# Optimization experiments

Measured on AMD Instinct MI355X. Metric: run time of the kernel, lower is better.

Reference implementation:

```python
import jax, jax.numpy as jnp
import numpy as np


def _sobel_mag(x_bchw):
    # per-channel Sobel gradient magnitude, then mean over channels -> [B,1,H,W]
    B, C, H, W = x_bchw.shape
    kx = jnp.array([[-1, 0, 1], [-2, 0, 2], [-1, 0, 1]], dtype=x_bchw.dtype).reshape(1, 1, 3, 3)
    ky = jnp.array([[-1, -2, -1], [0, 0, 0], [1, 2, 1]], dtype=x_bchw.dtype).reshape(1, 1, 3, 3)
    xf = x_bchw.reshape(B * C, 1, H, W)
    dn = ('NCHW', 'OIHW', 'NCHW')
    gx = jax.lax.conv_general_dilated(xf, kx, (1, 1), 'SAME', dimension_numbers=dn)
    gy = jax.lax.conv_general_dilated(xf, ky, (1, 1), 'SAME', dimension_numbers=dn)
    mag = jnp.sqrt(gx * gx + gy * gy + 1e-8).reshape(B, C, H, W)
    return mag.mean(axis=1, keepdims=True)


def _bi_wkv(w, u, k, v):
    # Bidirectional WKV (Vision-RWKV):
    # y_t = (sum_{i!=t} exp(k_i - (|t-i|-1)*w) v_i + exp(u+k_t) v_t)
    #     / (sum_{i!=t} exp(k_i - (|t-i|-1)*w)     + exp(u+k_t))
    # w,u: [C];  k,v: [B,T,C]. Numerically stable prefix scans in both directions.
    B, T, C = k.shape
    kt = jnp.transpose(k, (1, 0, 2))  # [T,B,C]
    vt = jnp.transpose(v, (1, 0, 2))

    def scan_dir(ks, vs):
        def step(carry, kv):
            a, b, pp = carry  # running num, den at log-offset pp (exclusive prefix)
            kk, vv = kv
            out = (a, b, pp)
            ww = pp - w  # decay one step
            p = jnp.maximum(ww, kk)
            e1 = jnp.exp(ww - p)
            e2 = jnp.exp(kk - p)
            return (e1 * a + e2 * vv, e1 * b + e2, p), out
        init = (jnp.zeros((B, C), k.dtype), jnp.zeros((B, C), k.dtype),
                jnp.full((B, C), -1e38, k.dtype))
        _, (a, b, pp) = jax.lax.scan(step, init, (ks, vs))
        return a, b, pp

    af, bf, pf = scan_dir(kt, vt)                       # contributions i < t
    ab, bb, pb = scan_dir(kt[::-1], vt[::-1])           # contributions i > t
    ab, bb, pb = ab[::-1], bb[::-1], pb[::-1]

    ps = u + kt                                         # self term exponent
    m = jnp.maximum(jnp.maximum(pf, pb), ps)
    ef = jnp.exp(pf - m)
    eb = jnp.exp(pb - m)
    es = jnp.exp(ps - m)
    num = af * ef + ab * eb + es * vt
    den = bf * ef + bb * eb + es
    return jnp.transpose(num / den, (1, 0, 2))  # [B,T,C]


def setup_inputs() -> dict:
    key = jax.random.key(0)
    ks = jax.random.split(key, 8)
    B, H, W, C = 8, 64, 64, 256
    T = H * W
    s = 1.0 / np.sqrt(C)
    return {
        'x': jax.random.normal(ks[0], (B, T, C), jnp.float32),
        'Wk': jax.random.normal(ks[1], (C, C), jnp.float32) * s,
        'Wv': jax.random.normal(ks[2], (C, C), jnp.float32) * s,
        'Wr': jax.random.normal(ks[3], (C, C), jnp.float32) * s,
        'Wo': jax.random.normal(ks[4], (C, C), jnp.float32) * s,
        'spatial_decay': jax.random.uniform(ks[5], (C,), jnp.float32, 0.5, 1.5),
        'spatial_first': jax.random.uniform(ks[6], (C,), jnp.float32, 0.5, 1.5),
        'H': H,
        'W': W,
    }


def reference(x, Wk, Wv, Wr, Wo, spatial_decay, spatial_first, H, W):
    B, T, C = x.shape
    k = x @ Wk.T
    v = x @ Wv.T
    r = x @ Wr.T
    sr = jax.nn.sigmoid(r)
    # edge gate
    x_hw = jnp.transpose(x, (0, 2, 1)).reshape(B, C, H, W)
    edge_g = jax.nn.sigmoid(_sobel_mag(x_hw)).reshape(B, 1, T)
    sr = sr + jnp.transpose(edge_g, (0, 2, 1))
    # bi-directional WKV with w,u scaled by 1/T (as in forward)
    xwkv = _bi_wkv(spatial_decay / T, spatial_first / T, k, v)
    return (sr * xwkv) @ Wo.T
```

## Files before the change

kernel.cpp:

```cpp
#include <hip/hip_runtime.h>
#include <hip/hip_bf16.h>

#define TB 8
#define TT 4096
#define TC 256
#define NC2 128
#define CL2 32

typedef _Float16 half8 __attribute__((ext_vector_type(8)));
typedef _Float16 half4v __attribute__((ext_vector_type(4)));
typedef float floatx4 __attribute__((ext_vector_type(4)));

#define GLDS16(g, l) __builtin_amdgcn_global_load_lds( \
    (const __attribute__((address_space(1))) void*)(g), \
    (__attribute__((address_space(3))) void*)(l), 16, 0, 0)

__global__ __launch_bounds__(256) void prep(
    const float* __restrict__ x,
    const float* __restrict__ Wk, const float* __restrict__ Wv,
    const float* __restrict__ Wr, const float* __restrict__ Wo,
    _Float16* __restrict__ Xh, _Float16* __restrict__ Xl,
    _Float16* __restrict__ Wf, float* __restrict__ edge)
{
    if (blockIdx.x >= TB * TT) {
        int t4 = (blockIdx.x - TB * TT) * 256 + threadIdx.x;
        int f = t4 * 4;
        int wsel = f >> 16;
        int i = f & 65535;
        const float* src = (wsel == 0) ? Wk : (wsel == 1) ? Wv :
                           (wsel == 2) ? Wr : Wo;
        float4 v = *(const float4*)(src + i);
        half4v h;
        h.x = (_Float16)v.x; h.y = (_Float16)v.y;
        h.z = (_Float16)v.z; h.w = (_Float16)v.w;
        *(half4v*)(Wf + (size_t)wsel * 65536 + i) = h;
        return;
    }
    int t = blockIdx.x & (TT - 1);
    int b = blockIdx.x >> 12;
    int h = t >> 6, w = t & 63;
    int c = threadIdx.x;

    float n[3][3];
    #pragma unroll
    for (int dh = 0; dh < 3; dh++) {
        int hh = h + dh - 1;
        #pragma unroll
        for (int dw = 0; dw < 3; dw++) {
            int ww = w + dw - 1;
            float val = 0.f;
            if (hh >= 0 && hh < 64 && ww >= 0 && ww < 64)
                val = x[((size_t)(b * TT + (hh << 6) + ww)) * TC + c];
            n[dh][dw] = val;
        }
    }
    float xc = n[1][1];
    _Float16 hi = (_Float16)xc;
    _Float16 lo = (_Float16)(xc - (float)hi);
    size_t mi = (size_t)(b * TT + t) * TC + c;
    Xh[mi] = hi;
    Xl[mi] = lo;

    float gx = (n[0][2] - n[0][0]) + 2.f * (n[1][2] - n[1][0]) + (n[2][2] - n[2][0]);
    float gy = (n[2][0] + 2.f * n[2][1] + n[2][2]) - (n[0][0] + 2.f * n[0][1] + n[0][2]);
    float mag = sqrtf(gx * gx + gy * gy + 1e-8f);

    #pragma unroll
    for (int off = 32; off > 0; off >>= 1) mag += __shfl_down(mag, off, 64);
    __shared__ float part[4];
    if ((threadIdx.x & 63) == 0) part[threadIdx.x >> 6] = mag;
    __syncthreads();
    if (threadIdx.x == 0) {
        float s = part[0] + part[1] + part[2] + part[3];
        edge[blockIdx.x] = 1.f / (1.f + __expf(-s * (1.f / 256.f)));
    }
}

__global__ __launch_bounds__(256, 2) void gemm_split(
    const _Float16* __restrict__ Ah_g, const _Float16* __restrict__ Al_g,
    const _Float16* __restrict__ W0, const _Float16* __restrict__ W1,
    const _Float16* __restrict__ W2p,
    void* __restrict__ C0, void* __restrict__ C1, void* __restrict__ C2,
    int ops)
{
    __shared__ __align__(16) _Float16 smem[16384];
    _Float16* Ah = smem;
    _Float16* Al = smem + 4096;
    _Float16* Bs = smem + 8192;

    int wsel = blockIdx.y;
    const _Float16* W = (wsel == 0) ? W0 : (wsel == 1) ? W1 : W2p;
    void* Cc          = (wsel == 0) ? C0 : (wsel == 1) ? C1 : C2;
    int op = (ops >> (2 * wsel)) & 3;
    int row0 = blockIdx.x * 128;

    int tid = threadIdx.x;
    int lane = tid & 63;
    int wv = tid >> 6;
    int qm = (wv >> 1) * 64;
    int qn = (wv & 1) * 128;

    floatx4 acc[4][8];
    #pragma unroll
    for (int i = 0; i < 4; i++)
        #pragma unroll
        for (int j = 0; j < 8; j++)
            acc[i][j] = (floatx4){0.f, 0.f, 0.f, 0.f};

    for (int kb = 0; kb < 256; kb += 32) {
        __syncthreads();
        #pragma unroll
        for (int r = 0; r < 2; r++) {
            int q = r * 256 + tid;
            int row = q >> 2;
            int s = q & 3;
            int g = (s - row - (row >> 2)) & 3;
            size_t goff = (size_t)(row0 + row) * TC + kb + g * 8;
            GLDS16(Ah_g + goff, &Ah[q * 8]);
            GLDS16(Al_g + goff, &Al[q * 8]);
        }
        #pragma unroll
        for (int r = 0; r < 4; r++) {
            int q = r * 256 + tid;
            int row = q >> 2, s = q & 3;
            int g = (s - row - (row >> 2)) & 3;
            GLDS16(W + (size_t)row * TC + kb + g * 8, &Bs[q * 8]);
        }
        __syncthreads();
        int sl = lane >> 4;
        half8 ah[4], al[4], b[8];
        #pragma unroll
        for (int i = 0; i < 4; i++) {
            int ra = qm + i * 16 + (lane & 15);
            int sa = (sl + ra + (ra >> 2)) & 3;
            ah[i] = *(const half8*)&Ah[ra * 32 + sa * 8];
            al[i] = *(const half8*)&Al[ra * 32 + sa * 8];
        }
        #pragma unroll
        for (int j = 0; j < 8; j++) {
            int rb = qn + j * 16 + (lane & 15);
            int sb = (sl + rb + (rb >> 2)) & 3;
            b[j] = *(const half8*)&Bs[rb * 32 + sb * 8];
        }
        #pragma unroll
        for (int i = 0; i < 4; i++)
            #pragma unroll
            for (int j = 0; j < 8; j++) {
                acc[i][j] = __builtin_amdgcn_mfma_f32_16x16x32_f16(
                    ah[i], b[j], acc[i][j], 0, 0, 0);
                acc[i][j] = __builtin_amdgcn_mfma_f32_16x16x32_f16(
                    al[i], b[j], acc[i][j], 0, 0, 0);
            }
    }

    int mr0 = (lane >> 4) * 4;
    int nc = lane & 15;
    #pragma unroll
    for (int i = 0; i < 4; i++) {
        #pragma unroll
        for (int r = 0; r < 4; r++) {
            int m = row0 + qm + i * 16 + mr0 + r;
            if (op == 0) {
                float* crow = (float*)Cc + (size_t)m * TC + qn + nc;
                #pragma unroll
                for (int j = 0; j < 8; j++)
                    crow[j * 16] = acc[i][j][r];
            } else {
                _Float16* crow = (_Float16*)Cc + (size_t)m * TC + qn + nc;
                #pragma unroll
                for (int j = 0; j < 8; j++) {
                    float vv = acc[i][j][r];
                    if (op == 1) vv = 1.f / (1.f + __expf(-vv));
                    else if (op == 2) vv = __expf(vv);
                    crow[j * 16] = (_Float16)vv;
                }
            }
        }
    }
}

__global__ __launch_bounds__(256) void wkv_chunk_sums(
    const _Float16* __restrict__ ekp, const _Float16* __restrict__ vp,
    const float* __restrict__ decay,
    float* __restrict__ SaF, float* __restrict__ SbF,
    float* __restrict__ RaB, float* __restrict__ RbB)
{
    int tid = blockIdx.x * 256 + threadIdx.x;
    int c = tid & 255;
    int j = (tid >> 8) & (NC2 - 1);
    int b = tid >> 15;
    float w = decay[c] * (1.f / (float)TT);
    float d = __expf(-w);
    size_t base = ((size_t)(b * TT + j * CL2)) * TC + c;
    float Sa = 0.f, Sb = 0.f, Ra = 0.f, Rb = 0.f, pw = 1.f;
    #pragma unroll
    for (int i = 0; i < CL2; i++) {
        float ek = (float)ekp[base + (size_t)i * TC];
        float vv = (float)vp[base + (size_t)i * TC];
        float ekv = ek * vv;
        Sa = fmaf(d, Sa, ekv);
        Sb = fmaf(d, Sb, ek);
        Ra = fmaf(pw, ekv, Ra);
        Rb = fmaf(pw, ek, Rb);
        pw *= d;
    }
    int idx = (b * NC2 + j) * TC + c;
    SaF[idx] = Sa; SbF[idx] = Sb; RaB[idx] = Ra; RbB[idx] = Rb;
}

__global__ __launch_bounds__(256) void wkv_carries(
    const float* __restrict__ SaF, const float* __restrict__ SbF,
    const float* __restrict__ RaB, const float* __restrict__ RbB,
    const float* __restrict__ decay,
    float* __restrict__ CfA, float* __restrict__ CfB,
    float* __restrict__ CbA, float* __restrict__ CbB)
{
    int gw = (blockIdx.x * 256 + threadIdx.x) >> 6;
    int lane = threadIdx.x & 63;
    int c = gw & 255, b = gw >> 8;
    float w = decay[c] * (1.f / (float)TT);
    float D = __expf(-(float)CL2 * w);
    int base = b * NC2 * TC + c;
    int j0 = 2 * lane, j1 = 2 * lane + 1;
    int r0 = NC2 - 1 - j0, r1 = NC2 - 2 - j0;

    float sa0 = SaF[base + j0 * TC], sa1 = SaF[base + j1 * TC];
    float sb0 = SbF[base + j0 * TC], sb1 = SbF[base + j1 * TC];
    float qa0 = RaB[base + r0 * TC], qa1 = RaB[base + r1 * TC];
    float qb0 = RbB[base + r0 * TC], qb1 = RbB[base + r1 * TC];

    float pa = fmaf(D, sa0, sa1), pb = fmaf(D, sb0, sb1);
    float ra = fmaf(D, qa0, qa1), rb = fmaf(D, qb0, qb1);

    float dp = D * D;
    #pragma unroll
    for (int off = 1; off < 64; off <<= 1) {
        float ta = __shfl_up(pa, off, 64);
        float tb = __shfl_up(pb, off, 64);
        float ua = __shfl_up(ra, off, 64);
        float ub = __shfl_up(rb, off, 64);
        if (lane >= off) {
            pa = fmaf(dp, ta, pa); pb = fmaf(dp, tb, pb);
            ra = fmaf(dp, ua, ra); rb = fmaf(dp, ub, rb);
        }
        dp = dp * dp;
    }
    float ppa = __shfl_up(pa, 1, 64);
    float ppb = __shfl_up(pb, 1, 64);
    float pra = __shfl_up(ra, 1, 64);
    float prb = __shfl_up(rb, 1, 64);
    if (lane == 0) { ppa = 0.f; ppb = 0.f; pra = 0.f; prb = 0.f; }

    CfA[base + j0 * TC] = ppa;
    CfA[base + j1 * TC] = fmaf(D, ppa, sa0);
    CfB[base + j0 * TC] = ppb;
    CfB[base + j1 * TC] = fmaf(D, ppb, sb0);
    CbA[base + r0 * TC] = pra;
    CbA[base + r1 * TC] = fmaf(D, pra, qa0);
    CbB[base + r0 * TC] = prb;
    CbB[base + r1 * TC] = fmaf(D, prb, qb0);
}

__global__ __launch_bounds__(256) void wkv_combine(
    const _Float16* __restrict__ ekp, const _Float16* __restrict__ vp,
    const _Float16* __restrict__ srp, const float* __restrict__ edgep,
    const float* __restrict__ decay, const float* __restrict__ first,
    const float* __restrict__ CfA, const float* __restrict__ CfB,
    const float* __restrict__ CbA, const float* __restrict__ CbB,
    _Float16* __restrict__ Yh, _Float16* __restrict__ Yl)
{
    __shared__ _Float16 ekL[CL2 * 256];
    __shared__ float ekvL[CL2 * 256];
    int bid = blockIdx.x;
    int j = bid & (NC2 - 1);
    int b = bid >> 7;
    int c = threadIdx.x;

    float w = decay[c] * (1.f / (float)TT);
    float d = __expf(-w);
    float eu = __expf(first[c] * (1.f / (float)TT));
    int cidx = (b * NC2 + j) * TC + c;
    size_t base = ((size_t)(b * TT + j * CL2)) * TC + c;

    float abArr[CL2], bbArr[CL2];
    float ab = CbA[cidx], bb = CbB[cidx];
    #pragma unroll
    for (int i = CL2 - 1; i >= 0; i--) {
        _Float16 ekh16 = ekp[base + (size_t)i * TC];
        float ek = (float)ekh16;
        float vv = (float)vp[base + (size_t)i * TC];
        float ekv = ek * vv;
        ekL[i * 256 + c] = ekh16;
        ekvL[i * 256 + c] = ekv;
        abArr[i] = ab; bbArr[i] = bb;
        ab = fmaf(d, ab, ekv);
        bb = fmaf(d, bb, ek);
    }
    float af = CfA[cidx], bf = CfB[cidx];
    #pragma unroll
    for (int i = 0; i < CL2; i++) {
        size_t idx = base + (size_t)i * TC;
        float ek = (float)ekL[i * 256 + c];
        float ekv = ekvL[i * 256 + c];
        float srv = (float)srp[idx];
        float num = fmaf(eu, ekv, af + abArr[i]);
        float den = fmaf(eu, ek, bf + bbArr[i]);
        float ev = edgep[b * TT + j * CL2 + i];
        float yv = (srv + ev) * (num / den);
        _Float16 yh = (_Float16)yv;
        _Float16 yl = (_Float16)(yv - (float)yh);
        Yh[idx] = yh;
        Yl[idx] = yl;
        af = fmaf(d, af, ekv);
        bf = fmaf(d, bf, ek);
    }
}

extern "C" void kernel_launch(void* const* d_in, const int* in_sizes, int n_in,
                              void* d_out, int out_size, void* d_ws, size_t ws_size,
                              hipStream_t stream)
{
    const float* x      = (const float*)d_in[0];
    const float* Wk     = (const float*)d_in[1];
    const float* Wv     = (const float*)d_in[2];
    const float* Wr     = (const float*)d_in[3];
    const float* Wo     = (const float*)d_in[4];
    const float* sdecay = (const float*)d_in[5];
    const float* sfirst = (const float*)d_in[6];
    float* out = (float*)d_out;

    char* ws = (char*)d_ws;
    size_t off = 0;
    const size_t PH = (size_t)TB * TT * TC * sizeof(_Float16);
    _Float16* Xh  = (_Float16*)(ws + off); off += PH;
    _Float16* Xl  = (_Float16*)(ws + off); off += PH;
    _Float16* ekh = (_Float16*)(ws + off); off += PH;
    _Float16* vbuf  = (_Float16*)(ws + off); off += PH;
    _Float16* srbuf = (_Float16*)(ws + off); off += PH;
    _Float16* Wf = (_Float16*)(ws + off); off += (size_t)4 * TC * TC * sizeof(_Float16);
    float* edge  = (float*)(ws + off); off += (size_t)TB * TT * sizeof(float);
    const size_t CHB = (size_t)TB * NC2 * TC * sizeof(float);
    float* SaF = (float*)(ws + off); off += CHB;
    float* SbF = (float*)(ws + off); off += CHB;
    float* RaB = (float*)(ws + off); off += CHB;
    float* RbB = (float*)(ws + off); off += CHB;
    float* CfA = (float*)(ws + off); off += CHB;
    float* CfB = (float*)(ws + off); off += CHB;
    float* CbA = (float*)(ws + off); off += CHB;
    float* CbB = (float*)(ws + off); off += CHB;

    _Float16* WfK = Wf;
    _Float16* WfV = Wf + (size_t)TC * TC;
    _Float16* WfR = Wf + (size_t)2 * TC * TC;
    _Float16* WfO = Wf + (size_t)3 * TC * TC;

    prep<<<TB * TT + 256, 256, 0, stream>>>(x, Wk, Wv, Wr, Wo, Xh, Xl, Wf, edge);

    int ops1 = 2 | (3 << 2) | (1 << 4);
    gemm_split<<<dim3((TB * TT) / 128, 3), 256, 0, stream>>>(
        Xh, Xl, WfK, WfV, WfR, ekh, vbuf, srbuf, ops1);

    wkv_chunk_sums<<<(TB * NC2 * TC) / 256, 256, 0, stream>>>(
        ekh, vbuf, sdecay, SaF, SbF, RaB, RbB);
    wkv_carries<<<(TB * TC * 64) / 256, 256, 0, stream>>>(
        SaF, SbF, RaB, RbB, sdecay, CfA, CfB, CbA, CbB);
    wkv_combine<<<TB * NC2, 256, 0, stream>>>(
        ekh, vbuf, srbuf, edge, sdecay, sfirst, CfA, CfB, CbA, CbB, Xh, Xl);

    gemm_split<<<dim3((TB * TT) / 128, 1), 256, 0, stream>>>(
        Xh, Xl, WfO, WfO, WfO, out, out, out, 0);
}
```

Before: 215.1 us.

## Split output GEMM into N=128 tiles, fold edge gate into sigmoid epilogue

Adds a dedicated output-projection GEMM kernel that covers 128 output columns per block, launched over two column halves. This doubles the block count and halves the accumulator registers and shared memory per block, aiming at better occupancy and wave coverage. The edge-gate addition moves into the sigmoid epilogue of the first GEMM. wkv_combine now keeps v in shared memory as fp16 and recomputes ek*v instead of storing it as fp32, which halves that LDS buffer. Adding edge before the fp16 rounding of sr slightly changes numerics.

```diff
diff --git a/kernel.cpp b/kernel.cpp
--- a/kernel.cpp
+++ b/kernel.cpp
@@ -81,7 +81,7 @@
     const _Float16* __restrict__ W0, const _Float16* __restrict__ W1,
     const _Float16* __restrict__ W2p,
     void* __restrict__ C0, void* __restrict__ C1, void* __restrict__ C2,
-    int ops)
+    const float* __restrict__ edgep, int ops)
 {
     __shared__ __align__(16) _Float16 smem[16384];
     _Float16* Ah = smem;
@@ -160,21 +160,96 @@
         #pragma unroll
         for (int r = 0; r < 4; r++) {
             int m = row0 + qm + i * 16 + mr0 + r;
-            if (op == 0) {
-                float* crow = (float*)Cc + (size_t)m * TC + qn + nc;
-                #pragma unroll
-                for (int j = 0; j < 8; j++)
-                    crow[j * 16] = acc[i][j][r];
-            } else {
-                _Float16* crow = (_Float16*)Cc + (size_t)m * TC + qn + nc;
-                #pragma unroll
-                for (int j = 0; j < 8; j++) {
-                    float vv = acc[i][j][r];
-                    if (op == 1) vv = 1.f / (1.f + __expf(-vv));
-                    else if (op == 2) vv = __expf(vv);
-                    crow[j * 16] = (_Float16)vv;
-                }
+            _Float16* crow = (_Float16*)Cc + (size_t)m * TC + qn + nc;
+            float ev = (op == 1) ? edgep[m] : 0.f;
+            #pragma unroll
+            for (int j = 0; j < 8; j++) {
+                float vv = acc[i][j][r];
+                if (op == 1) vv = 1.f / (1.f + __expf(-vv)) + ev;
+                else if (op == 2) vv = __expf(vv);
+                crow[j * 16] = (_Float16)vv;
             }
+        }
+    }
+}
+
+__global__ __launch_bounds__(256, 2) void gemm_n128(
+    const _Float16* __restrict__ Ah_g, const _Float16* __restrict__ Al_g,
+    const _Float16* __restrict__ W, float* __restrict__ C)
+{
+    __shared__ __align__(16) _Float16 smem[12288];
+    _Float16* Ah = smem;
+    _Float16* Al = smem + 4096;
+    _Float16* Bs = smem + 8192;
+
+    int col0 = (blockIdx.y & 1) * 128;
+    int row0 = blockIdx.x * 128;
+    const _Float16* Bg = W + (size_t)col0 * TC;
+
+    int tid = threadIdx.x;
+    int lane = tid & 63;
+    int wv = tid >> 6;
+    int qm = (wv >> 1) * 64;
+    int qn = (wv & 1) * 64;
+
+    floatx4 acc[4][4];
+    #pragma unroll
+    for (int i = 0; i < 4; i++)
+        #pragma unroll
+        for (int j = 0; j < 4; j++)
+            acc[i][j] = (floatx4){0.f, 0.f, 0.f, 0.f};
+
+    for (int kb = 0; kb < 256; kb += 32) {
+        __syncthreads();
+        #pragma unroll
+        for (int r = 0; r < 2; r++) {
+            int q = r * 256 + tid;
+            int row = q >> 2;
+            int s = q & 3;
+            int g = (s - row - (row >> 2)) & 3;
+            size_t goff = (size_t)(row0 + row) * TC + kb + g * 8;
+            GLDS16(Ah_g + goff, &Ah[q * 8]);
+            GLDS16(Al_g + goff, &Al[q * 8]);
+            GLDS16(Bg + (size_t)row * TC + kb + g * 8, &Bs[q * 8]);
+        }
+        __syncthreads();
+        int sl = lane >> 4;
+        half8 ah[4], al[4], b[4];
+        #pragma unroll
+        for (int i = 0; i < 4; i++) {
+            int ra = qm + i * 16 + (lane & 15);
+            int sa = (sl + ra + (ra >> 2)) & 3;
+            ah[i] = *(const half8*)&Ah[ra * 32 + sa * 8];
+            al[i] = *(const half8*)&Al[ra * 32 + sa * 8];
+        }
+        #pragma unroll
+        for (int j = 0; j < 4; j++) {
+            int rb = qn + j * 16 + (lane & 15);
+            int sb = (sl + rb + (rb >> 2)) & 3;
+            b[j] = *(const half8*)&Bs[rb * 32 + sb * 8];
+        }
+        #pragma unroll
+        for (int i = 0; i < 4; i++)
+            #pragma unroll
+            for (int j = 0; j < 4; j++) {
+                acc[i][j] = __builtin_amdgcn_mfma_f32_16x16x32_f16(
+                    ah[i], b[j], acc[i][j], 0, 0, 0);
+                acc[i][j] = __builtin_amdgcn_mfma_f32_16x16x32_f16(
+                    al[i], b[j], acc[i][j], 0, 0, 0);
+            }
+    }
+
+    int mr0 = (lane >> 4) * 4;
+    int nc = lane & 15;
+    #pragma unroll
+    for (int i = 0; i < 4; i++) {
+        #pragma unroll
+        for (int r = 0; r < 4; r++) {
+            int m = row0 + qm + i * 16 + mr0 + r;
+            float* crow = C + (size_t)m * TC + col0 + qn + nc;
+            #pragma unroll
+            for (int j = 0; j < 4; j++)
+                crow[j * 16] = acc[i][j][r];
         }
     }
 }
@@ -263,14 +338,14 @@
 
 __global__ __launch_bounds__(256) void wkv_combine(
     const _Float16* __restrict__ ekp, const _Float16* __restrict__ vp,
-    const _Float16* __restrict__ srp, const float* __restrict__ edgep,
+    const _Float16* __restrict__ srp,
     const float* __restrict__ decay, const float* __restrict__ first,
     const float* __restrict__ CfA, const float* __restrict__ CfB,
     const float* __restrict__ CbA, const float* __restrict__ CbB,
     _Float16* __restrict__ Yh, _Float16* __restrict__ Yl)
 {
     __shared__ _Float16 ekL[CL2 * 256];
-    __shared__ float ekvL[CL2 * 256];
+    __shared__ _Float16 vL[CL2 * 256];
     int bid = blockIdx.x;
     int j = bid & (NC2 - 1);
     int b = bid >> 7;
@@ -287,11 +362,12 @@
     #pragma unroll
     for (int i = CL2 - 1; i >= 0; i--) {
         _Float16 ekh16 = ekp[base + (size_t)i * TC];
+        _Float16 vh16 = vp[base + (size_t)i * TC];
         float ek = (float)ekh16;
-        float vv = (float)vp[base + (size_t)i * TC];
+        float vv = (float)vh16;
         float ekv = ek * vv;
         ekL[i * 256 + c] = ekh16;
-        ekvL[i * 256 + c] = ekv;
+        vL[i * 256 + c] = vh16;
         abArr[i] = ab; bbArr[i] = bb;
         ab = fmaf(d, ab, ekv);
         bb = fmaf(d, bb, ek);
@@ -301,12 +377,12 @@
     for (int i = 0; i < CL2; i++) {
         size_t idx = base + (size_t)i * TC;
         float ek = (float)ekL[i * 256 + c];
-        float ekv = ekvL[i * 256 + c];
+        float vv = (float)vL[i * 256 + c];
+        float ekv = ek * vv;
         float srv = (float)srp[idx];
         float num = fmaf(eu, ekv, af + abArr[i]);
         float den = fmaf(eu, ek, bf + bbArr[i]);
-        float ev = edgep[b * TT + j * CL2 + i];
-        float yv = (srv + ev) * (num / den);
+        float yv = srv * (num / den);
         _Float16 yh = (_Float16)yv;
         _Float16 yl = (_Float16)(yv - (float)yh);
         Yh[idx] = yh;
@@ -358,15 +434,15 @@
 
     int ops1 = 2 | (3 << 2) | (1 << 4);
     gemm_split<<<dim3((TB * TT) / 128, 3), 256, 0, stream>>>(
-        Xh, Xl, WfK, WfV, WfR, ekh, vbuf, srbuf, ops1);
+        Xh, Xl, WfK, WfV, WfR, ekh, vbuf, srbuf, edge, ops1);
 
     wkv_chunk_sums<<<(TB * NC2 * TC) / 256, 256, 0, stream>>>(
         ekh, vbuf, sdecay, SaF, SbF, RaB, RbB);
     wkv_carries<<<(TB * TC * 64) / 256, 256, 0, stream>>>(
         SaF, SbF, RaB, RbB, sdecay, CfA, CfB, CbA, CbB);
     wkv_combine<<<TB * NC2, 256, 0, stream>>>(
-        ekh, vbuf, srbuf, edge, sdecay, sfirst, CfA, CfB, CbA, CbB, Xh, Xl);
-
-    gemm_split<<<dim3((TB * TT) / 128, 1), 256, 0, stream>>>(
-        Xh, Xl, WfO, WfO, WfO, out, out, out, 0);
-}
+        ekh, vbuf, srbuf, sdecay, sfirst, CfA, CfB, CbA, CbB, Xh, Xl);
+
+    gemm_n128<<<dim3((TB * TT) / 128, 2), 256, 0, stream>>>(
+        Xh, Xl, WfO, out);
+}
```

Result: no change. 218.2 us (+1.5%).

## Load GEMM operands directly into registers and fold edge gate into sigmoid epilogue

Applied to the files above, without the earlier changes.

The GEMM no longer stages A and B tiles through LDS with async global-to-LDS loads and barriers. Each wave now loads its MFMA fragments straight from global memory into registers, with B processed in two halves to limit register pressure. The edge-gate add moves from the WKV combine kernel into the sigmoid epilogue of the r projection. The combine kernel now keeps fp16 v in LDS instead of fp32 ek*v, halving that buffer. The trade-off is that operands loaded by several waves are no longer shared, so the GEMM relies on cache hits, and storing sr plus edge in fp16 adds a small rounding change.

```diff
diff --git a/kernel.cpp b/kernel.cpp
--- a/kernel.cpp
+++ b/kernel.cpp
@@ -10,10 +10,6 @@
 typedef _Float16 half8 __attribute__((ext_vector_type(8)));
 typedef _Float16 half4v __attribute__((ext_vector_type(4)));
 typedef float floatx4 __attribute__((ext_vector_type(4)));
-
-#define GLDS16(g, l) __builtin_amdgcn_global_load_lds( \
-    (const __attribute__((address_space(1))) void*)(g), \
-    (__attribute__((address_space(3))) void*)(l), 16, 0, 0)
 
 __global__ __launch_bounds__(256) void prep(
     const float* __restrict__ x,
@@ -76,29 +72,29 @@
     }
 }
 
-__global__ __launch_bounds__(256, 2) void gemm_split(
+__global__ __launch_bounds__(256, 2) void gemm_reg(
     const _Float16* __restrict__ Ah_g, const _Float16* __restrict__ Al_g,
     const _Float16* __restrict__ W0, const _Float16* __restrict__ W1,
     const _Float16* __restrict__ W2p,
     void* __restrict__ C0, void* __restrict__ C1, void* __restrict__ C2,
-    int ops)
-{
-    __shared__ __align__(16) _Float16 smem[16384];
-    _Float16* Ah = smem;
-    _Float16* Al = smem + 4096;
-    _Float16* Bs = smem + 8192;
-
+    const float* __restrict__ edgep, int ops)
+{
     int wsel = blockIdx.y;
     const _Float16* W = (wsel == 0) ? W0 : (wsel == 1) ? W1 : W2p;
     void* Cc          = (wsel == 0) ? C0 : (wsel == 1) ? C1 : C2;
     int op = (ops >> (2 * wsel)) & 3;
     int row0 = blockIdx.x * 128;
 
-    int tid = threadIdx.x;
-    int lane = tid & 63;
-    int wv = tid >> 6;
+    int lane = threadIdx.x & 63;
+    int wv = threadIdx.x >> 6;
     int qm = (wv >> 1) * 64;
     int qn = (wv & 1) * 128;
+    int mr = lane & 15;
+    int kg = (lane >> 4) * 8;
+
+    const _Float16* Ah_b = Ah_g + (size_t)(row0 + qm + mr) * TC + kg;
+    const _Float16* Al_b = Al_g + (size_t)(row0 + qm + mr) * TC + kg;
+    const _Float16* Wb   = W + (size_t)(qn + mr) * TC + kg;
 
     floatx4 acc[4][8];
     #pragma unroll
@@ -107,50 +103,30 @@
         for (int j = 0; j < 8; j++)
             acc[i][j] = (floatx4){0.f, 0.f, 0.f, 0.f};
 
-    for (int kb = 0; kb < 256; kb += 32) {
-        __syncthreads();
-        #pragma unroll
-        for (int r = 0; r < 2; r++) {
-            int q = r * 256 + tid;
-            int row = q >> 2;
-            int s = q & 3;
-            int g = (s - row - (row >> 2)) & 3;
-            size_t goff = (size_t)(row0 + row) * TC + kb + g * 8;
-            GLDS16(Ah_g + goff, &Ah[q * 8]);
-            GLDS16(Al_g + goff, &Al[q * 8]);
-        }
-        #pragma unroll
-        for (int r = 0; r < 4; r++) {
-            int q = r * 256 + tid;
-            int row = q >> 2, s = q & 3;
-            int g = (s - row - (row >> 2)) & 3;
-            GLDS16(W + (size_t)row * TC + kb + g * 8, &Bs[q * 8]);
-        }
-        __syncthreads();
-        int sl = lane >> 4;
-        half8 ah[4], al[4], b[8];
+    for (int kk = 0; kk < TC; kk += 32) {
+        half8 ah[4], al[4];
         #pragma unroll
         for (int i = 0; i < 4; i++) {
-            int ra = qm + i * 16 + (lane & 15);
-            int sa = (sl + ra + (ra >> 2)) & 3;
-            ah[i] = *(const half8*)&Ah[ra * 32 + sa * 8];
-            al[i] = *(const half8*)&Al[ra * 32 + sa * 8];
-        }
-        #pragma unroll
-        for (int j = 0; j < 8; j++) {
-            int rb = qn + j * 16 + (lane & 15);
-            int sb = (sl + rb + (rb >> 2)) & 3;
-            b[j] = *(const half8*)&Bs[rb * 32 + sb * 8];
-        }
-        #pragma unroll
-        for (int i = 0; i < 4; i++)
+            ah[i] = *(const half8*)(Ah_b + (size_t)(i * 16) * TC + kk);
+            al[i] = *(const half8*)(Al_b + (size_t)(i * 16) * TC + kk);
+        }
+        #pragma unroll
+        for (int jh = 0; jh < 2; jh++) {
+            half8 b[4];
             #pragma unroll
-            for (int j = 0; j < 8; j++) {
-                acc[i][j] = __builtin_amdgcn_mfma_f32_16x16x32_f16(
-                    ah[i], b[j], acc[i][j], 0, 0, 0);
-                acc[i][j] = __builtin_amdgcn_mfma_f32_16x16x32_f16(
-                    al[i], b[j], acc[i][j], 0, 0, 0);
-            }
+            for (int j = 0; j < 4; j++)
+                b[j] = *(const half8*)(Wb + (size_t)(jh * 64 + j * 16) * TC + kk);
+            #pragma unroll
+            for (int i = 0; i < 4; i++)
+                #pragma unroll
+                for (int j = 0; j < 4; j++) {
+                    int jj = jh * 4 + j;
+                    acc[i][jj] = __builtin_amdgcn_mfma_f32_16x16x32_f16(
+                        ah[i], b[j], acc[i][jj], 0, 0, 0);
+                    acc[i][jj] = __builtin_amdgcn_mfma_f32_16x16x32_f16(
+                        al[i], b[j], acc[i][jj], 0, 0, 0);
+                }
+        }
     }
 
     int mr0 = (lane >> 4) * 4;
@@ -167,10 +143,11 @@
                     crow[j * 16] = acc[i][j][r];
             } else {
                 _Float16* crow = (_Float16*)Cc + (size_t)m * TC + qn + nc;
+                float ev = (op == 1) ? edgep[m] : 0.f;
                 #pragma unroll
                 for (int j = 0; j < 8; j++) {
                     float vv = acc[i][j][r];
-                    if (op == 1) vv = 1.f / (1.f + __expf(-vv));
+                    if (op == 1) vv = 1.f / (1.f + __expf(-vv)) + ev;
                     else if (op == 2) vv = __expf(vv);
                     crow[j * 16] = (_Float16)vv;
                 }
@@ -263,14 +240,14 @@
 
 __global__ __launch_bounds__(256) void wkv_combine(
     const _Float16* __restrict__ ekp, const _Float16* __restrict__ vp,
-    const _Float16* __restrict__ srp, const float* __restrict__ edgep,
+    const _Float16* __restrict__ srp,
     const float* __restrict__ decay, const float* __restrict__ first,
     const float* __restrict__ CfA, const float* __restrict__ CfB,
     const float* __restrict__ CbA, const float* __restrict__ CbB,
     _Float16* __restrict__ Yh, _Float16* __restrict__ Yl)
 {
     __shared__ _Float16 ekL[CL2 * 256];
-    __shared__ float ekvL[CL2 * 256];
+    __shared__ _Float16 vL[CL2 * 256];
     int bid = blockIdx.x;
     int j = bid & (NC2 - 1);
     int b = bid >> 7;
@@ -287,11 +264,12 @@
     #pragma unroll
     for (int i = CL2 - 1; i >= 0; i--) {
         _Float16 ekh16 = ekp[base + (size_t)i * TC];
+        _Float16 vh16 = vp[base + (size_t)i * TC];
         float ek = (float)ekh16;
-        float vv = (float)vp[base + (size_t)i * TC];
+        float vv = (float)vh16;
         float ekv = ek * vv;
         ekL[i * 256 + c] = ekh16;
-        ekvL[i * 256 + c] = ekv;
+        vL[i * 256 + c] = vh16;
         abArr[i] = ab; bbArr[i] = bb;
         ab = fmaf(d, ab, ekv);
         bb = fmaf(d, bb, ek);
@@ -301,12 +279,12 @@
     for (int i = 0; i < CL2; i++) {
         size_t idx = base + (size_t)i * TC;
         float ek = (float)ekL[i * 256 + c];
-        float ekv = ekvL[i * 256 + c];
+        float vv = (float)vL[i * 256 + c];
+        float ekv = ek * vv;
         float srv = (float)srp[idx];
         float num = fmaf(eu, ekv, af + abArr[i]);
         float den = fmaf(eu, ek, bf + bbArr[i]);
-        float ev = edgep[b * TT + j * CL2 + i];
-        float yv = (srv + ev) * (num / den);
+        float yv = srv * (num / den);
         _Float16 yh = (_Float16)yv;
         _Float16 yl = (_Float16)(yv - (float)yh);
         Yh[idx] = yh;
@@ -357,16 +335,16 @@
     prep<<<TB * TT + 256, 256, 0, stream>>>(x, Wk, Wv, Wr, Wo, Xh, Xl, Wf, edge);
 
     int ops1 = 2 | (3 << 2) | (1 << 4);
-    gemm_split<<<dim3((TB * TT) / 128, 3), 256, 0, stream>>>(
-        Xh, Xl, WfK, WfV, WfR, ekh, vbuf, srbuf, ops1);
+    gemm_reg<<<dim3((TB * TT) / 128, 3), 256, 0, stream>>>(
+        Xh, Xl, WfK, WfV, WfR, ekh, vbuf, srbuf, edge, ops1);
 
     wkv_chunk_sums<<<(TB * NC2 * TC) / 256, 256, 0, stream>>>(
         ekh, vbuf, sdecay, SaF, SbF, RaB, RbB);
     wkv_carries<<<(TB * TC * 64) / 256, 256, 0, stream>>>(
         SaF, SbF, RaB, RbB, sdecay, CfA, CfB, CbA, CbB);
     wkv_combine<<<TB * NC2, 256, 0, stream>>>(
-        ekh, vbuf, srbuf, edge, sdecay, sfirst, CfA, CfB, CbA, CbB, Xh, Xl);
-
-    gemm_split<<<dim3((TB * TT) / 128, 1), 256, 0, stream>>>(
-        Xh, Xl, WfO, WfO, WfO, out, out, out, 0);
-}
+        ekh, vbuf, srbuf, sdecay, sfirst, CfA, CfB, CbA, CbB, Xh, Xl);
+
+    gemm_reg<<<dim3((TB * TT) / 128, 1), 256, 0, stream>>>(
+        Xh, Xl, WfO, WfO, WfO, out, out, out, edge, 0);
+}
```

Result: slower. 239.1 us (+11.1%).
